# Optimization experiments

Measured on AMD Instinct MI355X. Metric: run time of the kernel, lower is better.

## Reference

```python
import jax, jax.numpy as jnp
import numpy as np

B, N, C = 8, 196, 512
NC, H = 10, 8
HD = C // H
SCALE = HD ** -0.5


def setup_inputs() -> dict:
    key = jax.random.key(0)
    ks = jax.random.split(key, 8)
    s = 1.0 / np.sqrt(C)
    return {
        "x": jax.random.normal(ks[0], (B, N, C), jnp.float32),
        "anchors": jax.random.normal(ks[1], (NC, N, C), jnp.float32),
        "weights": jax.random.uniform(ks[2], (B, H, NC), jnp.float32),
        "Wqk": jax.random.normal(ks[3], (C, C), jnp.float32) * s,
        "Wqk2": jax.random.normal(ks[4], (C, C), jnp.float32) * s,
        "Wv": jax.random.normal(ks[5], (C, C), jnp.float32) * s,
        "Wproj": jax.random.normal(ks[6], (C, C), jnp.float32) * s,
        "bproj": jax.random.normal(ks[7], (C,), jnp.float32) * 0.01,
    }


def _heads(t):
    # (..., N, C) -> (..., H, N, HD)
    shp = t.shape[:-2]
    return t.reshape(shp + (t.shape[-2], H, HD)).swapaxes(-3, -2)


def reference(x, anchors, weights, Wqk, Wqk2, Wv, Wproj, bproj):
    v = _heads(x @ Wv)                      # (B, H, N, HD)
    q = _heads(x @ Wqk)[:, None]            # (B, 1, H, N, HD)
    k = _heads(anchors @ Wqk)[None]         # (1, NC, H, N, HD)
    q2 = _heads(x @ Wqk2)[:, None]          # (B, 1, H, N, HD)
    k2 = _heads(anchors @ Wqk2)[None]       # (1, NC, H, N, HD)

    # ReLU-clipped double attention, both (B, NC, H, N, N)
    left_attn = jnp.maximum(-(q @ k.swapaxes(-2, -1)) * SCALE, 0.0)
    right_attn = jnp.maximum((k2 @ q2.swapaxes(-2, -1)) * SCALE, 0.0)

    attn = left_attn @ right_attn           # (B, NC, H, N, N)
    # per-head class-weighted combine: (B,H,NC) x (B,NC,H,N,N) -> (B,H,N,N)
    tmp = jnp.einsum('bhc,bchnm->bhnm', weights, attn)
    out = tmp @ v                           # (B, H, N, HD)
    # NOTE: original torch code reshapes (B,H,N,HD)->(B,N,C) WITHOUT a
    # transpose back; we replicate that exact flatten order.
    out = out.reshape(B, N, C)
    out = out @ Wproj + bproj
    return (out, left_attn)
```

## Files before the change

### kernel.cpp

```cpp
#include <hip/hip_runtime.h>

#define OFF_XB     0u
#define OFF_AB     1605632u
#define OFF_WQKT   3612672u
#define OFF_WQK2T  4136960u
#define OFF_WVT    4661248u
#define OFF_WPROJT 5185536u
#define OFF_XQ     5709824u
#define OFF_XQ2    7315456u
#define OFF_XV     8921088u
#define OFF_AQ     10526720u
#define OFF_AQ2    12533760u
#define OFF_RVT    14540800u
#define OFF_OUT1   35512320u
#define OFF_P      37117952u

typedef __attribute__((ext_vector_type(8))) short bf16x8;
typedef __attribute__((ext_vector_type(4))) float f32x4;
#define MFMA(a, b, c) __builtin_amdgcn_mfma_f32_16x16x32_bf16((a), (b), (c), 0, 0, 0)

__device__ __forceinline__ unsigned short f2bf(float x) {
  unsigned u = __builtin_bit_cast(unsigned, x);
  u += 0x7fffu + ((u >> 16) & 1u);
  return (unsigned short)(u >> 16);
}
__device__ __forceinline__ float bf2f(unsigned short s) {
  return __builtin_bit_cast(float, ((unsigned)s) << 16);
}

__device__ __forceinline__ void gl_lds16(const void* g, void* l) {
  __builtin_amdgcn_global_load_lds(
      (const __attribute__((address_space(1))) unsigned int*)g,
      (__attribute__((address_space(3))) unsigned int*)l, 16, 0, 0);
}

__device__ __forceinline__ void stage64(const unsigned short* g0, int stride,
                                        unsigned short (*T)[72], int tid, int nrows) {
  int wv = tid >> 6;
  char* base = (char*)&T[0][0];
#pragma unroll
  for (int i = 0; i < 2; i++) {
    int k = i * 256 + tid;
    int r = k / 9, c = k - r * 9;
    if (r < nrows)
      gl_lds16(g0 + (size_t)r * stride + (c << 3), base + (((i << 2) + wv) << 10));
  }
  if (tid < 64) {
    int k = 512 + tid;
    int r = k / 9, c = k - r * 9;
    if (r < nrows)
      gl_lds16(g0 + (size_t)r * stride + (c << 3), base + 8192);
  }
}

__device__ __forceinline__ void load_bf16_tile(unsigned short T[64][72], const unsigned short* __restrict__ g,
                                               int row0, int nrows, int col0, int tid) {
  int r = tid >> 2;
  int c0 = (tid & 3) << 4;
  uint4 a = make_uint4(0, 0, 0, 0), b = make_uint4(0, 0, 0, 0);
  if (r < nrows) {
    const unsigned short* p = g + (size_t)(row0 + r) * 512 + col0 + c0;
    a = *(const uint4*)p;
    b = *(const uint4*)(p + 8);
  }
  *(uint4*)&T[r][c0] = a;
  *(uint4*)&T[r][c0 + 8] = b;
}

__device__ __forceinline__ void vload_T(uint4* va, uint4* vb, const unsigned short* __restrict__ g,
                                        int row0, int nrows, int col0, int tid) {
  int j0 = tid >> 3, d0 = (tid & 7) << 3;
  *va = make_uint4(0, 0, 0, 0);
  *vb = make_uint4(0, 0, 0, 0);
  if (j0 < nrows) *va = *(const uint4*)(g + (size_t)(row0 + j0) * 512 + col0 + d0);
  if (j0 + 32 < nrows) *vb = *(const uint4*)(g + (size_t)(row0 + j0 + 32) * 512 + col0 + d0);
}
__device__ __forceinline__ void vwrite_T(unsigned short T[64][72], uint4 va, uint4 vb, int tid) {
  int j0 = tid >> 3, d0 = (tid & 7) << 3;
  unsigned short s[8];
  *(uint4*)s = va;
#pragma unroll
  for (int u = 0; u < 8; u++) T[d0 + u][j0] = s[u];
  *(uint4*)s = vb;
#pragma unroll
  for (int u = 0; u < 8; u++) T[d0 + u][j0 + 32] = s[u];
}

__global__ __launch_bounds__(256) void pre_kernel(const float* __restrict__ x, const float* __restrict__ anchors,
                                                  const float* __restrict__ Wqk, const float* __restrict__ Wqk2,
                                                  const float* __restrict__ Wv, const float* __restrict__ Wproj,
                                                  char* __restrict__ ws) {
  int tid = threadIdx.x;
  if (blockIdx.x < 1764) {
    int base = blockIdx.x * 1024 + (tid << 2);
    float4 f = (base < 802816) ? *(const float4*)(x + base)
                               : *(const float4*)(anchors + (base - 802816));
    unsigned short s[4] = {f2bf(f.x), f2bf(f.y), f2bf(f.z), f2bf(f.w)};
    *(uint2*)((unsigned short*)(ws + OFF_XB) + base) = *(uint2*)s;
    return;
  }
  __shared__ __align__(16) unsigned short Ls[64][72];
  int idx = blockIdx.x - 1764;
  int wsel = idx >> 6, t = idx & 63;
  int k0 = (t >> 3) << 6, n0 = (t & 7) << 6;
  const float* W;
  unsigned short* WT;
  switch (wsel) {
    case 0:  W = Wqk;   WT = (unsigned short*)(ws + OFF_WQKT);   break;
    case 1:  W = Wqk2;  WT = (unsigned short*)(ws + OFF_WQK2T);  break;
    case 2:  W = Wv;    WT = (unsigned short*)(ws + OFF_WVT);    break;
    default: W = Wproj; WT = (unsigned short*)(ws + OFF_WPROJT); break;
  }
  {
    int r = tid >> 2, seg = (tid & 3) << 4;
    const float* p = W + (size_t)(k0 + r) * 512 + n0 + seg;
    float4 f0 = *(const float4*)p, f1 = *(const float4*)(p + 4);
    float4 f2 = *(const float4*)(p + 8), f3 = *(const float4*)(p + 12);
    unsigned short s[16] = {f2bf(f0.x), f2bf(f0.y), f2bf(f0.z), f2bf(f0.w),
                            f2bf(f1.x), f2bf(f1.y), f2bf(f1.z), f2bf(f1.w),
                            f2bf(f2.x), f2bf(f2.y), f2bf(f2.z), f2bf(f2.w),
                            f2bf(f3.x), f2bf(f3.y), f2bf(f3.z), f2bf(f3.w)};
    *(uint4*)&Ls[r][seg] = *(uint4*)s;
    *(uint4*)&Ls[r][seg + 8] = *(uint4*)(s + 8);
  }
  __syncthreads();
  {
    int r = tid >> 2, seg = (tid & 3) << 4;
    unsigned short s[16];
#pragma unroll
    for (int u = 0; u < 16; u++) s[u] = Ls[seg + u][r];
    unsigned short* dst = WT + (size_t)(n0 + r) * 512 + k0 + seg;
    *(uint4*)dst = *(uint4*)s;
    *(uint4*)(dst + 8) = *(uint4*)(s + 8);
  }
}

template <bool STORE_BF16>
__device__ __forceinline__ void gemm_bf16_body(const unsigned short* __restrict__ A,
                                               const unsigned short* __restrict__ WT,
                                               const float* __restrict__ bias, void* __restrict__ outp,
                                               int M, int row_blk, int col_blk) {
  __shared__ __align__(16) unsigned short As[64][72];
  __shared__ __align__(16) unsigned short Ws[64][72];
  int row0 = row_blk << 6;
  if (row0 >= M) return;
  int col0 = col_blk << 6;
  int tid = threadIdx.x;
  int w = tid >> 6, lm = tid & 15, lq = (tid >> 4) & 3;
  f32x4 acc[4] = {};
  for (int k0 = 0; k0 < 512; k0 += 64) {
    __syncthreads();
    stage64(A + (size_t)row0 * 512 + k0, 512, As, tid, 64);
    stage64(WT + (size_t)col0 * 512 + k0, 512, Ws, tid, 64);
    __syncthreads();
#pragma unroll
    for (int kk = 0; kk < 2; kk++) {
      bf16x8 bf = *(const bf16x8*)&Ws[(w << 4) + lm][(kk << 5) + (lq << 3)];
#pragma unroll
      for (int mi = 0; mi < 4; mi++) {
        bf16x8 af = *(const bf16x8*)&As[(mi << 4) + lm][(kk << 5) + (lq << 3)];
        acc[mi] = MFMA(af, bf, acc[mi]);
      }
    }
  }
  int ncol = col0 + (w << 4) + lm;
  float bv = bias ? bias[ncol] : 0.f;
#pragma unroll
  for (int mi = 0; mi < 4; mi++)
#pragma unroll
    for (int r2 = 0; r2 < 4; r2++) {
      int row = row0 + (mi << 4) + (lq << 2) + r2;
      if (row < M) {
        if (STORE_BF16)
          ((unsigned short*)outp)[(size_t)row * 512 + ncol] = f2bf(acc[mi][r2]);
        else
          ((float*)outp)[(size_t)row * 512 + ncol] = acc[mi][r2] + bv;
      }
    }
}

__global__ __launch_bounds__(256) void proj5(char* __restrict__ ws) {
  const unsigned short* xb = (const unsigned short*)(ws + OFF_XB);
  const unsigned short* ab = (const unsigned short*)(ws + OFF_AB);
  const unsigned short* A; const unsigned short* WT; unsigned short* O; int M;
  switch (blockIdx.z) {
    case 0:  A = xb; WT = (unsigned short*)(ws + OFF_WQKT);  O = (unsigned short*)(ws + OFF_XQ);  M = 1568; break;
    case 1:  A = xb; WT = (unsigned short*)(ws + OFF_WQK2T); O = (unsigned short*)(ws + OFF_XQ2); M = 1568; break;
    case 2:  A = xb; WT = (unsigned short*)(ws + OFF_WVT);   O = (unsigned short*)(ws + OFF_XV);  M = 1568; break;
    case 3:  A = ab; WT = (unsigned short*)(ws + OFF_WQKT);  O = (unsigned short*)(ws + OFF_AQ);  M = 1960; break;
    default: A = ab; WT = (unsigned short*)(ws + OFF_WQK2T); O = (unsigned short*)(ws + OFF_AQ2); M = 1960; break;
  }
  gemm_bf16_body<true>(A, WT, nullptr, O, M, blockIdx.x, blockIdx.y);
}

__global__ __launch_bounds__(256) void final_gemm(const unsigned short* __restrict__ out1,
                                                  const unsigned short* __restrict__ WT,
                                                  const float* __restrict__ bias, float* __restrict__ out) {
  gemm_bf16_body<false>(out1, WT, bias, out, 1568, blockIdx.x, blockIdx.y);
}

__global__ __launch_bounds__(256) void rv_mfma(char* __restrict__ ws) {
  const unsigned short* xq2 = (const unsigned short*)(ws + OFF_XQ2);
  const unsigned short* aq2 = (const unsigned short*)(ws + OFF_AQ2);
  const unsigned short* xv  = (const unsigned short*)(ws + OFF_XV);
  unsigned short* rvt       = (unsigned short*)(ws + OFF_RVT);
  __shared__ __align__(16) unsigned short Ks[64][72];
  __shared__ __align__(16) unsigned short Qs[64][72];
  __shared__ __align__(16) unsigned short Vt[64][72];
  __shared__ __align__(16) unsigned short Ss[64][72];
  int i0 = blockIdx.x << 6;
  int bch = blockIdx.y;
  int h = bch & 7, bc = bch >> 3;
  int c = bc % 10, b = bc / 10;
  int tid = threadIdx.x;
  int w = tid >> 6, lm = tid & 15, lq = (tid >> 4) & 3;
  int ni = min(64, 196 - i0);

  load_bf16_tile(Ks, aq2, c * 196 + i0, ni, h << 6, tid);
  stage64(xq2 + (size_t)(b * 196) * 512 + (h << 6), 512, Qs, tid, 64);
  uint4 va, vb;
  vload_T(&va, &vb, xv, b * 196, 64, h << 6, tid);

  bf16x8 kb[2];
  f32x4 acc[4] = {};
#pragma unroll
  for (int jt = 0; jt < 4; jt++) {
    int j0 = jt << 6;
    __syncthreads();
    if (jt == 0) {
#pragma unroll
      for (int kk = 0; kk < 2; kk++)
        kb[kk] = *(const bf16x8*)&Ks[(w << 4) + lm][(kk << 5) + (lq << 3)];
    }
    vwrite_T(Vt, va, vb, tid);
    f32x4 s[4] = {};
#pragma unroll
    for (int kk = 0; kk < 2; kk++)
#pragma unroll
      for (int mj = 0; mj < 4; mj++) {
        bf16x8 af = *(const bf16x8*)&Qs[(mj << 4) + lm][(kk << 5) + (lq << 3)];
        s[mj] = MFMA(af, kb[kk], s[mj]);
      }
#pragma unroll
    for (int mj = 0; mj < 4; mj++) {
      unsigned short u[4] = {f2bf(fmaxf(0.125f * s[mj][0], 0.f)), f2bf(fmaxf(0.125f * s[mj][1], 0.f)),
                             f2bf(fmaxf(0.125f * s[mj][2], 0.f)), f2bf(fmaxf(0.125f * s[mj][3], 0.f))};
      *(uint2*)&Ss[(w << 4) + lm][(mj << 4) + (lq << 2)] = *(uint2*)u;
    }
    if (jt < 3) vload_T(&va, &vb, xv, b * 196 + j0 + 64, min(64, 196 - j0 - 64), h << 6, tid);
    __syncthreads();
    if (jt < 3) stage64(xq2 + (size_t)(b * 196 + j0 + 64) * 512 + (h << 6), 512, Qs, tid, 64);
#pragma unroll
    for (int kk = 0; kk < 2; kk++) {
      bf16x8 bf = *(const bf16x8*)&Vt[(w << 4) + lm][(kk << 5) + (lq << 3)];
#pragma unroll
      for (int mi = 0; mi < 4; mi++) {
        bf16x8 af = *(const bf16x8*)&Ss[(mi << 4) + lm][(kk << 5) + (lq << 3)];
        acc[mi] = MFMA(af, bf, acc[mi]);
      }
    }
  }
  __syncthreads();
#pragma unroll
  for (int mi = 0; mi < 4; mi++) {
    unsigned short u[4] = {f2bf(acc[mi][0]), f2bf(acc[mi][1]), f2bf(acc[mi][2]), f2bf(acc[mi][3])};
    *(uint2*)&Ss[(w << 4) + lm][(mi << 4) + (lq << 2)] = *(uint2*)u;
  }
  __syncthreads();
  {
    int dd = tid >> 2, seg = (tid & 3) << 4;
    unsigned short* dst = rvt + ((size_t)(bch * 4 + blockIdx.x) * 64 + dd) * 64 + seg;
    *(uint4*)dst = *(uint4*)&Ss[dd][seg];
    *(uint4*)(dst + 8) = *(uint4*)&Ss[dd][seg + 8];
  }
}

__global__ __launch_bounds__(256) void attn_mfma(char* __restrict__ ws, float* __restrict__ left,
                                                 unsigned short* __restrict__ P) {
  const unsigned short* xq  = (const unsigned short*)(ws + OFF_XQ);
  const unsigned short* aq  = (const unsigned short*)(ws + OFF_AQ);
  const unsigned short* rvt = (const unsigned short*)(ws + OFF_RVT);
  __shared__ __align__(16) unsigned short Qs[64][72];
  __shared__ __align__(16) unsigned short Ks[64][72];
  __shared__ __align__(16) unsigned short Ss[64][72];
  int i0 = blockIdx.x << 6;
  int bh = blockIdx.y;
  int c = blockIdx.z;
  int b = bh >> 3, h = bh & 7;
  int bch = (b * 10 + c) * 8 + h;
  int tid = threadIdx.x;
  int w = tid >> 6, lm = tid & 15, lq = (tid >> 4) & 3;

  stage64(xq + (size_t)(b * 196 + i0) * 512 + (h << 6), 512, Qs, tid, 64);
  {
    uint4 z = make_uint4(0, 0, 0, 0);
    for (int k = tid; k < 540; k += 256)
      *(uint4*)((char*)&Ks[0][0] + 576 + k * 16) = z;
  }
  stage64(aq + (size_t)(c * 196 + 192) * 512 + (h << 6), 512, Ks, tid, 4);

  bf16x8 qb[2];
  f32x4 acc[4] = {};
  size_t lbase = (size_t)bch * (196 * 196);
  int iglob = i0 + (w << 4) + lm;
#pragma unroll
  for (int t = 0; t < 4; t++) {
    int jt = (t == 0) ? 3 : t - 1;
    int j0 = jt << 6;
    __syncthreads();
    const unsigned short* rp = rvt + (size_t)(bch * 4 + jt) * 4096 + (((w << 4) + lm) << 6) + (lq << 3);
    bf16x8 rvb0 = *(const bf16x8*)rp;
    bf16x8 rvb1 = *(const bf16x8*)(rp + 32);
    if (t == 0) {
#pragma unroll
      for (int kk = 0; kk < 2; kk++)
        qb[kk] = *(const bf16x8*)&Qs[(w << 4) + lm][(kk << 5) + (lq << 3)];
    }
    f32x4 s[4] = {};
#pragma unroll
    for (int kk = 0; kk < 2; kk++)
#pragma unroll
      for (int mj = 0; mj < 4; mj++) {
        bf16x8 af = *(const bf16x8*)&Ks[(mj << 4) + lm][(kk << 5) + (lq << 3)];
        s[mj] = MFMA(af, qb[kk], s[mj]);
      }
#pragma unroll
    for (int mj = 0; mj < 4; mj++) {
      float4 lv;
      lv.x = fmaxf(-0.125f * s[mj][0], 0.f);
      lv.y = fmaxf(-0.125f * s[mj][1], 0.f);
      lv.z = fmaxf(-0.125f * s[mj][2], 0.f);
      lv.w = fmaxf(-0.125f * s[mj][3], 0.f);
      int jloc = (mj << 4) + (lq << 2);
      if (iglob < 196 && j0 + jloc < 196)
        *(float4*)&left[lbase + (size_t)iglob * 196 + j0 + jloc] = lv;
      unsigned short u[4] = {f2bf(lv.x), f2bf(lv.y), f2bf(lv.z), f2bf(lv.w)};
      *(uint2*)&Ss[(w << 4) + lm][jloc] = *(uint2*)u;
    }
    __syncthreads();
    if (t < 3)
      stage64(aq + (size_t)(c * 196 + (t << 6)) * 512 + (h << 6), 512, Ks, tid, 64);
#pragma unroll
    for (int kk = 0; kk < 2; kk++) {
      bf16x8 bf = (kk == 0) ? rvb0 : rvb1;
#pragma unroll
      for (int mi = 0; mi < 4; mi++) {
        bf16x8 af = *(const bf16x8*)&Ss[(mi << 4) + lm][(kk << 5) + (lq << 3)];
        acc[mi] = MFMA(af, bf, acc[mi]);
      }
    }
  }
  __syncthreads();
#pragma unroll
  for (int mi = 0; mi < 4; mi++)
#pragma unroll
    for (int r = 0; r < 4; r++)
      Ss[(mi << 4) + (lq << 2) + r][(w << 4) + lm] = f2bf(acc[mi][r]);
  __syncthreads();
  {
    int row = tid >> 2, seg = (tid & 3) << 4;
    if (i0 + row < 196) {
      unsigned short* dst = P + ((size_t)(bh * 10 + c) * 196 + i0 + row) * 64 + seg;
      *(uint4*)dst = *(uint4*)&Ss[row][seg];
      *(uint4*)(dst + 8) = *(uint4*)&Ss[row][seg + 8];
    }
  }
}

__global__ __launch_bounds__(256) void reduce_out1(const unsigned short* __restrict__ P,
                                                   const float* __restrict__ weights,
                                                   unsigned short* __restrict__ out1) {
  int t = blockIdx.x * 256 + threadIdx.x;
  int base = t << 2;
  int bh = base / 12544;
  int rem = base - bh * 12544;
  const float* wrow = weights + bh * 10;
  float a0 = 0.f, a1 = 0.f, a2 = 0.f, a3 = 0.f;
#pragma unroll
  for (int c = 0; c < 10; c++) {
    float wc = wrow[c];
    const unsigned short* p = P + ((size_t)(bh * 10 + c)) * 12544 + rem;
    ushort4 u = *(const ushort4*)p;
    a0 = fmaf(wc, bf2f(u.x), a0);
    a1 = fmaf(wc, bf2f(u.y), a1);
    a2 = fmaf(wc, bf2f(u.z), a2);
    a3 = fmaf(wc, bf2f(u.w), a3);
  }
  unsigned short s[4] = {f2bf(a0), f2bf(a1), f2bf(a2), f2bf(a3)};
  *(uint2*)&out1[base] = *(uint2*)s;
}

extern "C" void kernel_launch(void* const* d_in, const int* in_sizes, int n_in,
                              void* d_out, int out_size, void* d_ws, size_t ws_size,
                              hipStream_t stream) {
  (void)in_sizes; (void)n_in; (void)out_size; (void)ws_size;
  const float* x       = (const float*)d_in[0];
  const float* anchors = (const float*)d_in[1];
  const float* weights = (const float*)d_in[2];
  const float* Wqk     = (const float*)d_in[3];
  const float* Wqk2    = (const float*)d_in[4];
  const float* Wv      = (const float*)d_in[5];
  const float* Wproj   = (const float*)d_in[6];
  const float* bproj   = (const float*)d_in[7];
  char* ws = (char*)d_ws;
  float* out  = (float*)d_out;
  float* left = out + 802816;

  dim3 blk(256);
  pre_kernel<<<dim3(2020), blk, 0, stream>>>(x, anchors, Wqk, Wqk2, Wv, Wproj, ws);
  proj5<<<dim3(31, 8, 5), blk, 0, stream>>>(ws);
  rv_mfma<<<dim3(4, 640), blk, 0, stream>>>(ws);
  attn_mfma<<<dim3(4, 64, 10), blk, 0, stream>>>(ws, left, (unsigned short*)(ws + OFF_P));
  reduce_out1<<<dim3(784), blk, 0, stream>>>((const unsigned short*)(ws + OFF_P), weights,
                                             (unsigned short*)(ws + OFF_OUT1));
  final_gemm<<<dim3(25, 8), blk, 0, stream>>>((const unsigned short*)(ws + OFF_OUT1),
                                              (const unsigned short*)(ws + OFF_WPROJT), bproj, out);
}
```

Measured before the change: 232.4 us.

## Remap attention grids for XCD-aware L2 locality and load fragments directly

```diff
diff --git a/kernel.cpp b/kernel.cpp
--- a/kernel.cpp
+++ b/kernel.cpp
@@ -53,20 +53,6 @@
   }
 }
 
-__device__ __forceinline__ void load_bf16_tile(unsigned short T[64][72], const unsigned short* __restrict__ g,
-                                               int row0, int nrows, int col0, int tid) {
-  int r = tid >> 2;
-  int c0 = (tid & 3) << 4;
-  uint4 a = make_uint4(0, 0, 0, 0), b = make_uint4(0, 0, 0, 0);
-  if (r < nrows) {
-    const unsigned short* p = g + (size_t)(row0 + r) * 512 + col0 + c0;
-    a = *(const uint4*)p;
-    b = *(const uint4*)(p + 8);
-  }
-  *(uint4*)&T[r][c0] = a;
-  *(uint4*)&T[r][c0 + 8] = b;
-}
-
 __device__ __forceinline__ void vload_T(uint4* va, uint4* vb, const unsigned short* __restrict__ g,
                                         int row0, int nrows, int col0, int tid) {
   int j0 = tid >> 3, d0 = (tid & 7) << 3;
@@ -204,34 +190,36 @@
   const unsigned short* aq2 = (const unsigned short*)(ws + OFF_AQ2);
   const unsigned short* xv  = (const unsigned short*)(ws + OFF_XV);
   unsigned short* rvt       = (unsigned short*)(ws + OFF_RVT);
-  __shared__ __align__(16) unsigned short Ks[64][72];
   __shared__ __align__(16) unsigned short Qs[64][72];
   __shared__ __align__(16) unsigned short Vt[64][72];
   __shared__ __align__(16) unsigned short Ss[64][72];
-  int i0 = blockIdx.x << 6;
-  int bch = blockIdx.y;
-  int h = bch & 7, bc = bch >> 3;
-  int c = bc % 10, b = bc / 10;
+  int d = blockIdx.x;
+  int wk = ((d & 7) * 320) + (d >> 3);
+  int it = wk & 3;
+  int g = wk >> 2;
+  int bh = g / 10, c = g - bh * 10;
+  int b = bh >> 3, h = bh & 7;
+  int bch = (b * 10 + c) * 8 + h;
+  int i0 = it << 6;
   int tid = threadIdx.x;
   int w = tid >> 6, lm = tid & 15, lq = (tid >> 4) & 3;
-  int ni = min(64, 196 - i0);
-
-  load_bf16_tile(Ks, aq2, c * 196 + i0, ni, h << 6, tid);
+  int iglob = i0 + (w << 4) + lm;
+
+  bf16x8 kb[2] = {};
+  if (iglob < 196) {
+    const unsigned short* kp = aq2 + (size_t)(c * 196 + iglob) * 512 + (h << 6) + (lq << 3);
+    kb[0] = *(const bf16x8*)kp;
+    kb[1] = *(const bf16x8*)(kp + 32);
+  }
   stage64(xq2 + (size_t)(b * 196) * 512 + (h << 6), 512, Qs, tid, 64);
   uint4 va, vb;
   vload_T(&va, &vb, xv, b * 196, 64, h << 6, tid);
 
-  bf16x8 kb[2];
   f32x4 acc[4] = {};
 #pragma unroll
   for (int jt = 0; jt < 4; jt++) {
     int j0 = jt << 6;
     __syncthreads();
-    if (jt == 0) {
-#pragma unroll
-      for (int kk = 0; kk < 2; kk++)
-        kb[kk] = *(const bf16x8*)&Ks[(w << 4) + lm][(kk << 5) + (lq << 3)];
-    }
     vwrite_T(Vt, va, vb, tid);
     f32x4 s[4] = {};
 #pragma unroll
@@ -269,7 +257,7 @@
   __syncthreads();
   {
     int dd = tid >> 2, seg = (tid & 3) << 4;
-    unsigned short* dst = rvt + ((size_t)(bch * 4 + blockIdx.x) * 64 + dd) * 64 + seg;
+    unsigned short* dst = rvt + ((size_t)(bch * 4 + it) * 64 + dd) * 64 + seg;
     *(uint4*)dst = *(uint4*)&Ss[dd][seg];
     *(uint4*)(dst + 8) = *(uint4*)&Ss[dd][seg + 8];
   }
@@ -280,42 +268,43 @@
   const unsigned short* xq  = (const unsigned short*)(ws + OFF_XQ);
   const unsigned short* aq  = (const unsigned short*)(ws + OFF_AQ);
   const unsigned short* rvt = (const unsigned short*)(ws + OFF_RVT);
-  __shared__ __align__(16) unsigned short Qs[64][72];
   __shared__ __align__(16) unsigned short Ks[64][72];
   __shared__ __align__(16) unsigned short Ss[64][72];
-  int i0 = blockIdx.x << 6;
-  int bh = blockIdx.y;
-  int c = blockIdx.z;
+  int d = blockIdx.x;
+  int wk = ((d & 7) * 320) + (d >> 3);
+  int i0 = (wk & 3) << 6;
+  int g = wk >> 2;
+  int c = g >> 6;
+  int bh = g & 63;
   int b = bh >> 3, h = bh & 7;
   int bch = (b * 10 + c) * 8 + h;
   int tid = threadIdx.x;
   int w = tid >> 6, lm = tid & 15, lq = (tid >> 4) & 3;
-
-  stage64(xq + (size_t)(b * 196 + i0) * 512 + (h << 6), 512, Qs, tid, 64);
+  int iglob = i0 + (w << 4) + lm;
+
+  bf16x8 qb[2];
+  {
+    const unsigned short* qp = xq + (size_t)(b * 196 + iglob) * 512 + (h << 6) + (lq << 3);
+    qb[0] = *(const bf16x8*)qp;
+    qb[1] = *(const bf16x8*)(qp + 32);
+  }
   {
     uint4 z = make_uint4(0, 0, 0, 0);
     for (int k = tid; k < 540; k += 256)
       *(uint4*)((char*)&Ks[0][0] + 576 + k * 16) = z;
   }
   stage64(aq + (size_t)(c * 196 + 192) * 512 + (h << 6), 512, Ks, tid, 4);
-
-  bf16x8 qb[2];
+  const unsigned short* rbase = rvt + (size_t)bch * 16384 + (((w << 4) + lm) << 6) + (lq << 3);
+  bf16x8 rv0 = *(const bf16x8*)(rbase + 3 * 4096);
+  bf16x8 rv1 = *(const bf16x8*)(rbase + 3 * 4096 + 32);
+
   f32x4 acc[4] = {};
   size_t lbase = (size_t)bch * (196 * 196);
-  int iglob = i0 + (w << 4) + lm;
 #pragma unroll
   for (int t = 0; t < 4; t++) {
     int jt = (t == 0) ? 3 : t - 1;
     int j0 = jt << 6;
     __syncthreads();
-    const unsigned short* rp = rvt + (size_t)(bch * 4 + jt) * 4096 + (((w << 4) + lm) << 6) + (lq << 3);
-    bf16x8 rvb0 = *(const bf16x8*)rp;
-    bf16x8 rvb1 = *(const bf16x8*)(rp + 32);
-    if (t == 0) {
-#pragma unroll
-      for (int kk = 0; kk < 2; kk++)
-        qb[kk] = *(const bf16x8*)&Qs[(w << 4) + lm][(kk << 5) + (lq << 3)];
-    }
     f32x4 s[4] = {};
 #pragma unroll
     for (int kk = 0; kk < 2; kk++)
@@ -326,23 +315,28 @@
       }
 #pragma unroll
     for (int mj = 0; mj < 4; mj++) {
-      float4 lv;
-      lv.x = fmaxf(-0.125f * s[mj][0], 0.f);
-      lv.y = fmaxf(-0.125f * s[mj][1], 0.f);
-      lv.z = fmaxf(-0.125f * s[mj][2], 0.f);
-      lv.w = fmaxf(-0.125f * s[mj][3], 0.f);
+      f32x4 lv;
+      lv[0] = fmaxf(-0.125f * s[mj][0], 0.f);
+      lv[1] = fmaxf(-0.125f * s[mj][1], 0.f);
+      lv[2] = fmaxf(-0.125f * s[mj][2], 0.f);
+      lv[3] = fmaxf(-0.125f * s[mj][3], 0.f);
       int jloc = (mj << 4) + (lq << 2);
       if (iglob < 196 && j0 + jloc < 196)
-        *(float4*)&left[lbase + (size_t)iglob * 196 + j0 + jloc] = lv;
-      unsigned short u[4] = {f2bf(lv.x), f2bf(lv.y), f2bf(lv.z), f2bf(lv.w)};
+        __builtin_nontemporal_store(lv, (f32x4*)&left[lbase + (size_t)iglob * 196 + j0 + jloc]);
+      unsigned short u[4] = {f2bf(lv[0]), f2bf(lv[1]), f2bf(lv[2]), f2bf(lv[3])};
       *(uint2*)&Ss[(w << 4) + lm][jloc] = *(uint2*)u;
     }
     __syncthreads();
     if (t < 3)
       stage64(aq + (size_t)(c * 196 + (t << 6)) * 512 + (h << 6), 512, Ks, tid, 64);
+    bf16x8 cur0 = rv0, cur1 = rv1;
+    if (t < 3) {
+      rv0 = *(const bf16x8*)(rbase + t * 4096);
+      rv1 = *(const bf16x8*)(rbase + t * 4096 + 32);
+    }
 #pragma unroll
     for (int kk = 0; kk < 2; kk++) {
-      bf16x8 bf = (kk == 0) ? rvb0 : rvb1;
+      bf16x8 bf = (kk == 0) ? cur0 : cur1;
 #pragma unroll
       for (int mi = 0; mi < 4; mi++) {
         bf16x8 af = *(const bf16x8*)&Ss[(mi << 4) + lm][(kk << 5) + (lq << 3)];
@@ -409,8 +403,8 @@
   dim3 blk(256);
   pre_kernel<<<dim3(2020), blk, 0, stream>>>(x, anchors, Wqk, Wqk2, Wv, Wproj, ws);
   proj5<<<dim3(31, 8, 5), blk, 0, stream>>>(ws);
-  rv_mfma<<<dim3(4, 640), blk, 0, stream>>>(ws);
-  attn_mfma<<<dim3(4, 64, 10), blk, 0, stream>>>(ws, left, (unsigned short*)(ws + OFF_P));
+  rv_mfma<<<dim3(2560), blk, 0, stream>>>(ws);
+  attn_mfma<<<dim3(2560), blk, 0, stream>>>(ws, left, (unsigned short*)(ws + OFF_P));
   reduce_out1<<<dim3(784), blk, 0, stream>>>((const unsigned short*)(ws + OFF_P), weights,
                                              (unsigned short*)(ws + OFF_OUT1));
   final_gemm<<<dim3(25, 8), blk, 0, stream>>>((const unsigned short*)(ws + OFF_OUT1),
```

Result: slower. 267.0 us (+14.9%).
